# Kernel tuning notes

Hardware: AMD Instinct MI355X
Metric: run time of the kernel (lower is better)

Reference implementation:

```python
import jax, jax.numpy as jnp
from jax import lax
import numpy as np

BN_EPS = 1e-3

def _hard_sigmoid(x):
    # Keras hard_sigmoid: relu6(x + 3) / 6
    return jnp.clip(x / 6.0 + 0.5, 0.0, 1.0)

def _conv(x, w):
    # x: [B,H,W,C], w: [kh,kw,C,Cout]
    return lax.conv_general_dilated(x, w, window_strides=(1, 1), padding='SAME',
                                    dimension_numbers=('NHWC', 'HWIO', 'NHWC'))

def _convlstm(x, Wx, Wh, b):
    # x: [B,T,H,W,C] -> [B,T,H,W,F]; gates packed i,f,c,o along last dim (Keras order)
    B, T, H, W, C = x.shape
    F = b.shape[0] // 4
    h0 = jnp.zeros((B, H, W, F), x.dtype)
    c0 = jnp.zeros_like(h0)

    def step(carry, xt):
        h, c = carry
        z = _conv(xt, Wx) + _conv(h, Wh) + b  # [B,H,W,4F]
        i, f, g, o = jnp.split(z, 4, axis=-1)
        c = _hard_sigmoid(f) * c + _hard_sigmoid(i) * jnp.tanh(g)
        h = _hard_sigmoid(o) * jnp.tanh(c)
        return (h, c), h

    _, hs = lax.scan(step, (h0, c0), jnp.moveaxis(x, 1, 0))  # [T,B,H,W,F]
    return jnp.moveaxis(hs, 0, 1)


def setup_inputs() -> dict:
    key = jax.random.key(0)
    ks = jax.random.split(key, 8)
    B, T, H, W, C, F = 4, 16, 64, 64, 48, 48
    x = jax.random.normal(ks[0], (B, T, H, W, C), jnp.float32)
    s = 0.05  # keep gate pre-activations in a sane range
    Wx1 = jax.random.normal(ks[1], (3, 3, C, 4 * F), jnp.float32) * s
    Wh1 = jax.random.normal(ks[2], (3, 3, F, 4 * F), jnp.float32) * s
    b1 = jax.random.normal(ks[3], (4 * F,), jnp.float32) * s
    Wx2 = jax.random.normal(ks[4], (3, 3, F, 4 * F), jnp.float32) * s
    Wh2 = jax.random.normal(ks[5], (3, 3, F, 4 * F), jnp.float32) * s
    b2 = jax.random.normal(ks[6], (4 * F,), jnp.float32) * s
    gamma = jnp.ones((F,), jnp.float32)
    beta = jnp.zeros((F,), jnp.float32)
    mean = jax.random.normal(ks[7], (F,), jnp.float32) * 0.1
    var = jax.random.uniform(jax.random.fold_in(key, 99), (F,), jnp.float32, 0.5, 1.5)
    return {"x": x, "Wx1": Wx1, "Wh1": Wh1, "b1": b1,
            "Wx2": Wx2, "Wh2": Wh2, "b2": b2,
            "gamma": gamma, "beta": beta, "mean": mean, "var": var}


def reference(x, Wx1, Wh1, b1, Wx2, Wh2, b2, gamma, beta, mean, var):
    h = _convlstm(x, Wx1, Wh1, b1)
    # Dropout(0.2) at inference: identity. BatchNorm (inference, per-channel):
    h = gamma * (h - mean) * lax.rsqrt(var + BN_EPS) + beta
    h = _convlstm(h, Wx2, Wh2, b2)
    return x + h  # channels match (C == filters) -> direct residual add
```

## Files before the change

### kernel.cpp

```cpp
#include <hip/hip_runtime.h>
#include <hip/hip_bf16.h>

typedef __bf16 bf16;
typedef __bf16 bf16x8 __attribute__((ext_vector_type(8)));
typedef float  f32x4  __attribute__((ext_vector_type(4)));
typedef unsigned short u16x8 __attribute__((ext_vector_type(8)));
typedef unsigned long long u64;

#define NB 4
#define NT 16
#define NH 64
#define NW 64
#define NC 48
#define RSTR 104
#define RKY  (66*RSTR)

__device__ __forceinline__ float hsig(float x){
    return fminf(fmaxf(x*0.16666667f + 0.5f, 0.0f), 1.0f);
}
__device__ __forceinline__ float ftanh(float x){
    float ax = fabsf(x);
    float e  = __expf(-2.0f*ax);
    float r  = (1.0f - e) * __builtin_amdgcn_rcpf(1.0f + e);
    return __builtin_copysignf(r, x);
}

__global__ void detect_dtype(const unsigned* __restrict__ g, int* __restrict__ flag){
    if (threadIdx.x == 0 && blockIdx.x == 0)
        *flag = (g[0] == 0x3F803F80u) ? 1 : 0;
}

__device__ __forceinline__ float ld_any(const void* p, int i, int isbf){
    return isbf ? (float)((const bf16*)p)[i] : ((const float*)p)[i];
}

__global__ void prep_weights(const void* __restrict__ Wx, const void* __restrict__ Wh,
                             const int* __restrict__ flag, bf16* __restrict__ Wsw){
    int isbf = *flag;
    int idx = blockIdx.x*256 + threadIdx.x;
    if (idx >= 165888) return;
    int e    = idx & 7;
    int lane = (idx >> 3) & 63;
    int nt   = (idx >> 9) % 12;
    int krk  = idx / (512*12);
    int ky = krk / 9, kr = krk % 9;
    int ln = lane & 15, lg = lane >> 4;
    int n_new  = nt*16 + ln;
    int gate = n_new & 3, c = n_new >> 2;
    int n_orig = gate*48 + c;
    int k  = kr*32 + lg*8 + e;
    int kx = k / 96, ch = k % 96;
    float v = (ch < 48) ? ld_any(Wx, ((ky*3+kx)*48 + ch)*192 + n_orig, isbf)
                        : ld_any(Wh, ((ky*3+kx)*48 + (ch-48))*192 + n_orig, isbf);
    Wsw[idx] = (bf16)v;
}

__global__ void prep_params(const void* b1, const void* b2, const void* gamma,
                            const void* beta, const void* mean, const void* var,
                            const int* __restrict__ flag, float* __restrict__ P){
    int isbf = *flag;
    int i = blockIdx.x*64 + threadIdx.x;
    if (i < 192)      P[i] = ld_any(b1, i, isbf);
    else if (i < 384) P[i] = ld_any(b2, i-192, isbf);
    else if (i < 432){
        int c = i-384;
        P[i] = ld_any(gamma,c,isbf) * rsqrtf(ld_any(var,c,isbf) + 1e-3f);
    } else if (i < 480){
        int c = i-432;
        float sc = ld_any(gamma,c,isbf) * rsqrtf(ld_any(var,c,isbf) + 1e-3f);
        P[i] = ld_any(beta,c,isbf) - ld_any(mean,c,isbf)*sc;
    }
}

__global__ __launch_bounds__(512, 1)
void fused_kernel(const void* __restrict__ x,
                  bf16* __restrict__ seq,
                  bf16* __restrict__ hA,
                  bf16* __restrict__ hB,
                  const bf16* __restrict__ Wc1,
                  const bf16* __restrict__ Wc2,
                  const float* __restrict__ P,
                  void* __restrict__ outp,
                  const int* __restrict__ flag,
                  int* __restrict__ done)
{
    __shared__ bf16  rowpad[3*RKY];
    __shared__ float zbuf[64*196];
    const int isbf = *flag;
    const int tid  = threadIdx.x;
    const int xcd  = blockIdx.x & 7;
    const int slot = blockIdx.x >> 3;
    const int img  = xcd >> 1;
    const int y    = ((xcd & 1) << 5) | slot;
    const int lane = tid & 63;
    const int wv   = tid >> 6;
    const int wn   = wv & 3;
    const int wg   = wv >> 2;
    const int ln   = lane & 15;
    const int lg   = lane >> 4;

    int* dme  = done + img*NH + y;
    int* dimg = done + img*NH;

    if (tid < 78){
        int ky = tid/26; int rmd = tid%26;
        int col = (rmd < 13) ? 0 : 65; int q = rmd % 13;
        u16x8 z = {};
        *(u16x8*)(rowpad + ky*RKY + col*RSTR + q*8) = z;
    }

    float creg[6];

    #pragma unroll 1
    for (int L = 0; L < 2; ++L){
        const bf16*  Wsw = L ? Wc2 : Wc1;
        const float* Pb  = P + (L ? 192 : 0);
        const void*  xs  = L ? (const void*)seq : x;
        const int    Loff = L*16;

        float bi_[3], bf_[3], bg_[3], bo_[3], bns[3], bnb[3];
        #pragma unroll
        for (int q = 0; q < 3; ++q){
            int cq = (tid + q*32) % 48;
            bi_[q] = Pb[cq];      bf_[q] = Pb[48+cq];
            bg_[q] = Pb[96+cq];   bo_[q] = Pb[144+cq];
            bns[q] = P[384+cq];   bnb[q] = P[432+cq];
        }

        auto stage_x = [&](int tt){
            for (int task = tid; task < 1152; task += 512){
                int ky = task/384, chn = task%384;
                int xcol = chn/6, c0 = (chn%6)*8;
                int row = y + ky - 1;
                u16x8 val = {};
                if (row >= 0 && row < NH){
                    int si = (((img*NT + tt)*NH + row)*NW + xcol)*NC + c0;
                    if (L == 1){
                        union { u16x8 v; u64 q[2]; } u;
                        u64* sp = (u64*)((const bf16*)xs + si);
                        u.q[0] = __hip_atomic_load(sp,   __ATOMIC_RELAXED, __HIP_MEMORY_SCOPE_AGENT);
                        u.q[1] = __hip_atomic_load(sp+1, __ATOMIC_RELAXED, __HIP_MEMORY_SCOPE_AGENT);
                        val = u.v;
                    } else if (isbf){
                        val = *(const u16x8*)((const bf16*)xs + si);
                    } else {
                        const float* src = (const float*)xs + si;
                        float4 f0 = *(const float4*)(src);
                        float4 f1 = *(const float4*)(src + 4);
                        bf16x8 v;
                        v[0]=(bf16)f0.x; v[1]=(bf16)f0.y; v[2]=(bf16)f0.z; v[3]=(bf16)f0.w;
                        v[4]=(bf16)f1.x; v[5]=(bf16)f1.y; v[6]=(bf16)f1.z; v[7]=(bf16)f1.w;
                        val = *(u16x8*)&v;
                    }
                }
                *(u16x8*)(rowpad + ky*RKY + (xcol+1)*RSTR + c0) = val;
            }
        };

        f32x4 acc[2][3];
        auto zero_acc = [&]{
            #pragma unroll
            for (int mt = 0; mt < 2; ++mt)
                #pragma unroll
                for (int j = 0; j < 3; ++j)
                    acc[mt][j] = (f32x4){0.f,0.f,0.f,0.f};
        };
        auto mfma_iter = [&](int ky, int kr){
            const bf16* wp = Wsw + (size_t)((ky*9 + kr)*12 + wn*3)*512 + lane*8;
            bf16x8 b0 = *(const bf16x8*)(wp);
            bf16x8 b1 = *(const bf16x8*)(wp + 512);
            bf16x8 b2 = *(const bf16x8*)(wp + 1024);
            const bf16* ap = rowpad + ky*RKY + (ln + (kr/3) + wg*32)*RSTR
                           + (kr%3)*32 + lg*8;
            #pragma unroll
            for (int mt = 0; mt < 2; ++mt){
                bf16x8 a = *(const bf16x8*)(ap + mt*16*RSTR);
                acc[mt][0] = __builtin_amdgcn_mfma_f32_16x16x32_bf16(a, b0, acc[mt][0], 0,0,0);
                acc[mt][1] = __builtin_amdgcn_mfma_f32_16x16x32_bf16(a, b1, acc[mt][1], 0,0,0);
                acc[mt][2] = __builtin_amdgcn_mfma_f32_16x16x32_bf16(a, b2, acc[mt][2], 0,0,0);
            }
        };
        auto groupA = [&]{
            #pragma unroll
            for (int kr = 0; kr < 9; ++kr) mfma_iter(1, kr);
            #pragma unroll
            for (int kx = 0; kx < 3; ++kx){ mfma_iter(0, kx*3); mfma_iter(2, kx*3); }
        };
        auto groupB = [&]{
            #pragma unroll
            for (int kx = 0; kx < 3; ++kx){
                mfma_iter(0, kx*3+1); mfma_iter(0, kx*3+2);
                mfma_iter(2, kx*3+1); mfma_iter(2, kx*3+2);
            }
        };

        stage_x(0);
        for (int task = tid; task < 1152; task += 512){
            int ky = task/384, chn = task%384;
            int xcol = chn/6, c0 = (chn%6)*8;
            u16x8 z = {};
            *(u16x8*)(rowpad + ky*RKY + (xcol+1)*RSTR + 48 + c0) = z;
        }
        #pragma unroll
        for (int i = 0; i < 6; ++i) creg[i] = 0.f;
        __syncthreads();

        zero_acc();
        groupA(); groupB();

        #pragma unroll 1
        for (int t = 0; t < NT; ++t){
            bf16* hw = ((t + L) & 1) ? hB : hA;

            #pragma unroll
            for (int mt = 0; mt < 2; ++mt)
                #pragma unroll
                for (int j = 0; j < 3; ++j)
                    #pragma unroll
                    for (int r = 0; r < 4; ++r)
                        zbuf[(wg*32 + mt*16 + lg*4 + r)*196 + wn*48 + j*16 + ln]
                            = acc[mt][j][r];
            __syncthreads();

            if (t < NT-1) stage_x(t+1);

            #pragma unroll
            for (int it = 0; it < 6; ++it){
                const int q = it % 3;
                int cell = tid + it*512;
                int pos = cell/48;
                int c = cell - pos*48;
                f32x4 z = *(const f32x4*)(zbuf + pos*196 + c*4);
                float cn = hsig(z[1]+bf_[q])*creg[it] + hsig(z[0]+bi_[q])*ftanh(z[2]+bg_[q]);
                float hn = hsig(z[3]+bo_[q])*ftanh(cn);
                creg[it] = cn;
                if (t < NT-1){
                    int gi = ((img*NH + y)*NW + pos)*NC + c;
                    hw[gi] = (bf16)hn;
                }
                rowpad[RKY + (pos+1)*RSTR + 48 + c] = (bf16)hn;
                int sidx = (((img*NT + t)*NH + y)*NW + pos)*NC + c;
                if (L == 0){
                    seq[sidx] = (bf16)(hn*bns[q] + bnb[q]);
                } else {
                    float xr = isbf ? (float)((const bf16*)x)[sidx]
                                    : ((const float*)x)[sidx];
                    float v = xr + hn;
                    if (isbf) ((bf16*)outp)[sidx] = (bf16)v;
                    else      ((float*)outp)[sidx] = v;
                }
            }

            __syncthreads();
            if (tid == 0)
                __hip_atomic_store(dme, Loff + t + 1,
                                   __ATOMIC_RELEASE, __HIP_MEMORY_SCOPE_AGENT);

            if (t < NT-1){
                zero_acc();
                groupA();

                if (tid < 2){
                    int nb = tid ? y+1 : y-1;
                    if (nb >= 0 && nb < NH){
                        const int need = Loff + t + 1;
                        while (__hip_atomic_load(dimg + nb, __ATOMIC_RELAXED,
                                                 __HIP_MEMORY_SCOPE_AGENT) < need)
                            __builtin_amdgcn_s_sleep(1);
                    }
                }
                __syncthreads();
                for (int task = tid; task < 768; task += 512){
                    int kyh = task/384;
                    int chn = task%384;
                    int ky  = kyh << 1;
                    int xcol = chn/6, c0 = (chn%6)*8;
                    int row = y + ky - 1;
                    union { u16x8 v; u64 q[2]; } u;
                    u.q[0] = 0; u.q[1] = 0;
                    if (row >= 0 && row < NH){
                        u64* hp = (u64*)(hw + ((img*NH + row)*NW + xcol)*NC + c0);
                        u.q[0] = __hip_atomic_load(hp,   __ATOMIC_RELAXED, __HIP_MEMORY_SCOPE_AGENT);
                        u.q[1] = __hip_atomic_load(hp+1, __ATOMIC_RELAXED, __HIP_MEMORY_SCOPE_AGENT);
                    }
                    *(u16x8*)(rowpad + ky*RKY + (xcol+1)*RSTR + 48 + c0) = u.v;
                }
                __syncthreads();

                groupB();
            }
        }
    }
}

extern "C" void kernel_launch(void* const* d_in, const int* in_sizes, int n_in,
                              void* d_out, int out_size, void* d_ws, size_t ws_size,
                              hipStream_t stream)
{
    const void* x     = d_in[0];
    const void* Wx1   = d_in[1];
    const void* Wh1   = d_in[2];
    const void* b1    = d_in[3];
    const void* Wx2   = d_in[4];
    const void* Wh2   = d_in[5];
    const void* b2    = d_in[6];
    const void* gamma = d_in[7];
    const void* beta  = d_in[8];
    const void* mean  = d_in[9];
    const void* var   = d_in[10];

    char* p = (char*)d_ws;
    auto carve = [&](size_t bytes)->void*{
        void* q = (void*)p; p += (bytes + 255) & ~(size_t)255; return q;
    };
    const size_t planeN = (size_t)NB*NH*NW*NC;
    int*   flag = (int*)  carve(256);
    float* P    = (float*)carve(480*sizeof(float));
    bf16*  Wc1  = (bf16*) carve(165888*sizeof(bf16));
    bf16*  Wc2  = (bf16*) carve(165888*sizeof(bf16));
    bf16*  hA   = (bf16*) carve(planeN*sizeof(bf16));
    bf16*  hB   = (bf16*) carve(planeN*sizeof(bf16));
    bf16*  seq  = (bf16*) carve((size_t)NB*NT*NH*NW*NC*sizeof(bf16));
    int*   done = (int*)  carve(NB*NH*sizeof(int));

    detect_dtype<<<1, 64, 0, stream>>>((const unsigned*)gamma, flag);
    prep_weights<<<648, 256, 0, stream>>>(Wx1, Wh1, flag, Wc1);
    prep_weights<<<648, 256, 0, stream>>>(Wx2, Wh2, flag, Wc2);
    prep_params<<<8, 64, 0, stream>>>(b1, b2, gamma, beta, mean, var, flag, P);
    hipMemsetAsync(done, 0, NB*NH*sizeof(int), stream);

    fused_kernel<<<dim3(NB*NH), dim3(512), 0, stream>>>(
        x, seq, hA, hB, Wc1, Wc2, P, d_out, flag, done);
}
```

Before: 554.8 us.

## Double block to 1024 threads and split gate N-tiles unevenly across 16 waves

Each block now runs 16 wavefronts instead of 8. The 12 N-tiles of gate outputs are spread over 8 waves per M-group: four waves take two tiles each and four take one. The elementwise LSTM update loop drops from 6 to 3 cells per thread. The aim is more latency hiding and more concurrent MFMA issue within the single persistent block per CU. In exchange, the wave tile split is unbalanced, each wave re-reads the A operand from LDS, and the register budget per thread is halved.

After: 1.258 ms. 2.27x slower.

```diff
diff --git a/kernel.cpp b/kernel.cpp
--- a/kernel.cpp
+++ b/kernel.cpp
@@ -72,7 +72,7 @@
     }
 }
 
-__global__ __launch_bounds__(512, 1)
+__global__ __launch_bounds__(1024, 1)
 void fused_kernel(const void* __restrict__ x,
                   bf16* __restrict__ seq,
                   bf16* __restrict__ hA,
@@ -94,8 +94,10 @@
     const int y    = ((xcd & 1) << 5) | slot;
     const int lane = tid & 63;
     const int wv   = tid >> 6;
-    const int wn   = wv & 3;
-    const int wg   = wv >> 2;
+    const int wg   = wv >> 3;
+    const int wwn  = wv & 7;
+    const int nt0  = (wwn < 4) ? 2*wwn : 8 + (wwn - 4);
+    const bool two = (wwn < 4);
     const int ln   = lane & 15;
     const int lg   = lane >> 4;
 
@@ -109,7 +111,7 @@
         *(u16x8*)(rowpad + ky*RKY + col*RSTR + q*8) = z;
     }
 
-    float creg[6];
+    float creg[3];
 
     #pragma unroll 1
     for (int L = 0; L < 2; ++L){
@@ -121,14 +123,14 @@
         float bi_[3], bf_[3], bg_[3], bo_[3], bns[3], bnb[3];
         #pragma unroll
         for (int q = 0; q < 3; ++q){
-            int cq = (tid + q*32) % 48;
+            int cq = (tid + q*16) % 48;
             bi_[q] = Pb[cq];      bf_[q] = Pb[48+cq];
             bg_[q] = Pb[96+cq];   bo_[q] = Pb[144+cq];
             bns[q] = P[384+cq];   bnb[q] = P[432+cq];
         }
 
         auto stage_x = [&](int tt){
-            for (int task = tid; task < 1152; task += 512){
+            for (int task = tid; task < 1152; task += 1024){
                 int ky = task/384, chn = task%384;
                 int xcol = chn/6, c0 = (chn%6)*8;
                 int row = y + ky - 1;
@@ -157,27 +159,27 @@
             }
         };
 
-        f32x4 acc[2][3];
+        f32x4 acc[2][2];
         auto zero_acc = [&]{
             #pragma unroll
             for (int mt = 0; mt < 2; ++mt)
                 #pragma unroll
-                for (int j = 0; j < 3; ++j)
+                for (int j = 0; j < 2; ++j)
                     acc[mt][j] = (f32x4){0.f,0.f,0.f,0.f};
         };
         auto mfma_iter = [&](int ky, int kr){
-            const bf16* wp = Wsw + (size_t)((ky*9 + kr)*12 + wn*3)*512 + lane*8;
+            const bf16* wp = Wsw + (size_t)((ky*9 + kr)*12 + nt0)*512 + lane*8;
             bf16x8 b0 = *(const bf16x8*)(wp);
-            bf16x8 b1 = *(const bf16x8*)(wp + 512);
-            bf16x8 b2 = *(const bf16x8*)(wp + 1024);
             const bf16* ap = rowpad + ky*RKY + (ln + (kr/3) + wg*32)*RSTR
                            + (kr%3)*32 + lg*8;
-            #pragma unroll
-            for (int mt = 0; mt < 2; ++mt){
-                bf16x8 a = *(const bf16x8*)(ap + mt*16*RSTR);
-                acc[mt][0] = __builtin_amdgcn_mfma_f32_16x16x32_bf16(a, b0, acc[mt][0], 0,0,0);
-                acc[mt][1] = __builtin_amdgcn_mfma_f32_16x16x32_bf16(a, b1, acc[mt][1], 0,0,0);
-                acc[mt][2] = __builtin_amdgcn_mfma_f32_16x16x32_bf16(a, b2, acc[mt][2], 0,0,0);
+            bf16x8 a0 = *(const bf16x8*)(ap);
+            bf16x8 a1 = *(const bf16x8*)(ap + 16*RSTR);
+            acc[0][0] = __builtin_amdgcn_mfma_f32_16x16x32_bf16(a0, b0, acc[0][0], 0,0,0);
+            acc[1][0] = __builtin_amdgcn_mfma_f32_16x16x32_bf16(a1, b0, acc[1][0], 0,0,0);
+            if (two){
+                bf16x8 b1 = *(const bf16x8*)(wp + 512);
+                acc[0][1] = __builtin_amdgcn_mfma_f32_16x16x32_bf16(a0, b1, acc[0][1], 0,0,0);
+                acc[1][1] = __builtin_amdgcn_mfma_f32_16x16x32_bf16(a1, b1, acc[1][1], 0,0,0);
             }
         };
         auto groupA = [&]{
@@ -193,16 +195,26 @@
                 mfma_iter(2, kx*3+1); mfma_iter(2, kx*3+2);
             }
         };
+        auto zwrite = [&]{
+            #pragma unroll
+            for (int mt = 0; mt < 2; ++mt)
+                #pragma unroll
+                for (int r = 0; r < 4; ++r){
+                    int row = wg*32 + mt*16 + lg*4 + r;
+                    zbuf[row*196 + nt0*16 + ln] = acc[mt][0][r];
+                    if (two) zbuf[row*196 + (nt0+1)*16 + ln] = acc[mt][1][r];
+                }
+        };
 
         stage_x(0);
-        for (int task = tid; task < 1152; task += 512){
+        for (int task = tid; task < 1152; task += 1024){
             int ky = task/384, chn = task%384;
             int xcol = chn/6, c0 = (chn%6)*8;
             u16x8 z = {};
             *(u16x8*)(rowpad + ky*RKY + (xcol+1)*RSTR + 48 + c0) = z;
         }
         #pragma unroll
-        for (int i = 0; i < 6; ++i) creg[i] = 0.f;
+        for (int i = 0; i < 3; ++i) creg[i] = 0.f;
         __syncthreads();
 
         zero_acc();
@@ -212,27 +224,19 @@
         for (int t = 0; t < NT; ++t){
             bf16* hw = ((t + L) & 1) ? hB : hA;
 
-            #pragma unroll
-            for (int mt = 0; mt < 2; ++mt)
-                #pragma unroll
-                for (int j = 0; j < 3; ++j)
-                    #pragma unroll
-                    for (int r = 0; r < 4; ++r)
-                        zbuf[(wg*32 + mt*16 + lg*4 + r)*196 + wn*48 + j*16 + ln]
-                            = acc[mt][j][r];
+            zwrite();
             __syncthreads();
 
             if (t < NT-1) stage_x(t+1);
 
             #pragma unroll
-            for (int it = 0; it < 6; ++it){
-                const int q = it % 3;
-                int cell = tid + it*512;
+            for (int it = 0; it < 3; ++it){
+                int cell = tid + it*1024;
                 int pos = cell/48;
                 int c = cell - pos*48;
                 f32x4 z = *(const f32x4*)(zbuf + pos*196 + c*4);
-                float cn = hsig(z[1]+bf_[q])*creg[it] + hsig(z[0]+bi_[q])*ftanh(z[2]+bg_[q]);
-                float hn = hsig(z[3]+bo_[q])*ftanh(cn);
+                float cn = hsig(z[1]+bf_[it])*creg[it] + hsig(z[0]+bi_[it])*ftanh(z[2]+bg_[it]);
+                float hn = hsig(z[3]+bo_[it])*ftanh(cn);
                 creg[it] = cn;
                 if (t < NT-1){
                     int gi = ((img*NH + y)*NW + pos)*NC + c;
@@ -241,7 +245,7 @@
                 rowpad[RKY + (pos+1)*RSTR + 48 + c] = (bf16)hn;
                 int sidx = (((img*NT + t)*NH + y)*NW + pos)*NC + c;
                 if (L == 0){
-                    seq[sidx] = (bf16)(hn*bns[q] + bnb[q]);
+                    seq[sidx] = (bf16)(hn*bns[it] + bnb[it]);
                 } else {
                     float xr = isbf ? (float)((const bf16*)x)[sidx]
                                     : ((const float*)x)[sidx];
@@ -270,7 +274,7 @@
                     }
                 }
                 __syncthreads();
-                for (int task = tid; task < 768; task += 512){
+                for (int task = tid; task < 768; task += 1024){
                     int kyh = task/384;
                     int chn = task%384;
                     int ky  = kyh << 1;
@@ -329,6 +333,6 @@
     prep_params<<<8, 64, 0, stream>>>(b1, b2, gamma, beta, mean, var, flag, P);
     hipMemsetAsync(done, 0, NB*NH*sizeof(int), stream);
 
-    fused_kernel<<<dim3(NB*NH), dim3(512), 0, stream>>>(
+    fused_kernel<<<dim3(NB*NH), dim3(1024), 0, stream>>>(
         x, seq, hA, hB, Wc1, Wc2, P, d_out, flag, done);
 }
```
